# Optimization experiments

Measured on AMD Instinct MI355X. Metric: run time of the kernel, lower is better.

Reference implementation:

```python
import jax, jax.numpy as jnp
import numpy as np

K = 32          # neighbors per point (SelectorConfig)
N_DEG = 3       # radial polynomial degree
L_DEG = 3       # theta degree
M_DEG = 3       # phi degree
NP = 16384
CI = 64
CO = 64
EPS = 1e-8


def setup_inputs() -> dict:
    key = jax.random.key(0)
    k1, k2, k3 = jax.random.split(key, 3)
    position_matrix = jax.random.normal(k1, (NP, 3), dtype=jnp.float32)
    channel_matrix = jax.random.normal(k2, (NP, CI), dtype=jnp.float32)
    B = N_DEG * L_DEG * M_DEG
    coeff = jax.random.normal(k3, (B, CI, CO), dtype=jnp.float32) * 0.05
    return {"position_matrix": position_matrix,
            "channel_matrix": channel_matrix,
            "coeff": coeff}


def _knn_indices(pos):
    # brute-force kNN: (Np, Np) squared distances, top-K smallest
    sq = jnp.sum(pos * pos, axis=1)
    d2 = sq[:, None] + sq[None, :] - 2.0 * (pos @ pos.T)  # (Np, Np)
    _, idx = jax.lax.top_k(-d2, K)                        # (Np, K), includes self
    return idx


def _local_spherical(pos, idx, use_pca=True):
    nbr = pos[idx]                                  # (Np, K, 3) gather
    centers = jnp.mean(nbr, axis=1, keepdims=True)  # (Np, 1, 3)
    local = nbr - centers                           # (Np, K, 3)
    cov = jnp.einsum('nki,nkj->nij', local, local) / K   # (Np, 3, 3)
    eigvals, eigvecs = jnp.linalg.eigh(cov)         # ascending
    eigvals = eigvals[:, ::-1]                      # descending
    eigvecs = eigvecs[:, :, ::-1]
    if use_pca:
        local = jnp.einsum('nki,nij->nkj', local, eigvecs)  # rotate into PCA frame
    x, y, z = local[..., 0], local[..., 1], local[..., 2]
    r = jnp.sqrt(jnp.sum(local * local, axis=-1) + EPS)     # (Np, K)
    theta = jnp.arccos(jnp.clip(z / r, -1.0 + 1e-6, 1.0 - 1e-6))
    phi = jnp.arctan2(y, x)
    return r, theta, phi, centers, eigvals


def _poly_basis(r, theta, phi):
    # basis[n,k,b] = r^i * cos(j*theta) * cos(m*phi),  b = (i,j,m) flattened
    pr = r[..., None] ** jnp.arange(N_DEG, dtype=r.dtype)              # (Np,K,N)
    ct = jnp.cos(theta[..., None] * jnp.arange(L_DEG, dtype=r.dtype))  # (Np,K,L)
    cp = jnp.cos(phi[..., None] * jnp.arange(M_DEG, dtype=r.dtype))    # (Np,K,M)
    basis = jnp.einsum('nka,nkb,nkc->nkabc', pr, ct, cp)
    return basis.reshape(r.shape[0], r.shape[1], N_DEG * L_DEG * M_DEG)


def reference(position_matrix, channel_matrix, coeff):
    idx = _knn_indices(position_matrix)                   # (Np, K)
    r, theta, phi, _, _ = _local_spherical(position_matrix, idx, use_pca=True)
    basis = _poly_basis(r, theta, phi)                    # (Np, K, B)
    feats = channel_matrix[idx]                           # (Np, K, Ci) gather
    # fused kernel-weight construction + weighted aggregation:
    # out[o,n] = (1/K) * sum_{k,b,i} basis[n,k,b] * coeff[b,i,o] * feats[n,k,i]
    out = jnp.einsum('nkb,bio,nki->on', basis, coeff, feats) / K  # (Co, Np)
    return out
```

## Files before the change

kernel.cpp:

```cpp
#include <hip/hip_runtime.h>
#include <math.h>

#define NPOINTS 16384
#define KNN     32
#define NBASIS  27

typedef unsigned long long ull;


__device__ __forceinline__ unsigned fkey(float f) {
  unsigned u = __float_as_uint(f);
  unsigned m = (unsigned)((int)u >> 31) | 0x80000000u;
  return u ^ m;
}

__device__ __forceinline__ ull shflx64(ull v, int mask) {
  int lo = __shfl_xor((int)(unsigned)(v & 0xFFFFFFFFULL), mask, 64);
  int hi = __shfl_xor((int)(unsigned)(v >> 32), mask, 64);
  return ((ull)(unsigned)hi << 32) | (ull)(unsigned)lo;
}

__device__ __forceinline__ unsigned prefix64(ull m) {
  return __builtin_amdgcn_mbcnt_hi((unsigned)(m >> 32),
         __builtin_amdgcn_mbcnt_lo((unsigned)m, 0u));
}


__device__ __forceinline__ void slartg_dev(double f, double g, double* c, double* s, double* r) {
#pragma clang fp contract(off)
  if (g == 0.0) { *c = 1.0; *s = 0.0; *r = f; }
  else if (f == 0.0) { *c = 0.0; *s = (g >= 0.0 ? 1.0 : -1.0); *r = fabs(g); }
  else {
    double d = sqrt(f * f + g * g);
    *c = fabs(f) / d;
    *r = (f >= 0.0) ? d : -d;
    *s = g / (*r);
  }
}

__device__ __forceinline__ void slaev2_dev(double a, double b, double c,
                                           double* rt1, double* rt2, double* cs1, double* sn1) {
#pragma clang fp contract(off)
  double sm = a + c, df = a - c, adf = fabs(df), tb = b + b, ab = fabs(tb);
  double acmx, acmn;
  if (fabs(a) > fabs(c)) { acmx = a; acmn = c; } else { acmx = c; acmn = a; }
  double rt;
  if (adf > ab)      rt = adf * sqrt(1.0 + (ab / adf) * (ab / adf));
  else if (adf < ab) rt = ab * sqrt(1.0 + (adf / ab) * (adf / ab));
  else               rt = ab * sqrt(2.0);
  int sgn1;
  if (sm < 0.0) { *rt1 = 0.5 * (sm - rt); sgn1 = -1; *rt2 = (acmx / *rt1) * acmn - (b / *rt1) * b; }
  else if (sm > 0.0) { *rt1 = 0.5 * (sm + rt); sgn1 = 1; *rt2 = (acmx / *rt1) * acmn - (b / *rt1) * b; }
  else { *rt1 = 0.5 * rt; *rt2 = -0.5 * rt; sgn1 = 1; }
  int sgn2; double cs;
  if (df >= 0.0) { cs = df + rt; sgn2 = 1; } else { cs = df - rt; sgn2 = -1; }
  double acs = fabs(cs);
  if (acs > ab) { double ct = -tb / cs; double sn = 1.0 / sqrt(1.0 + ct * ct); *sn1 = sn; *cs1 = ct * sn; }
  else {
    if (ab == 0.0) { *cs1 = 1.0; *sn1 = 0.0; }
    else { double tn = -cs / tb; double c1 = 1.0 / sqrt(1.0 + tn * tn); *cs1 = c1; *sn1 = tn * c1; }
  }
  if (sgn1 == sgn2) { double tn = *cs1; *cs1 = -(*sn1); *sn1 = tn; }
}

__device__ void eigh3(float A00, float A10, float A20, float A11, float A21, float A22,
                      float V[3][3]) {
#pragma clang fp contract(off)
  const double EPS    = 5.9604644775390625e-08;
  const double EPS2   = EPS * EPS;
  const double SAFMIN = 1.1754943508222875e-38;
  double d[3], e[2];
  double tau = 0.0, v2 = 0.0;
  {
    double alpha = (double)A10, x = (double)A20;
    double a11 = (double)A11, a21 = (double)A21, a22 = (double)A22;
    double beta;
    if (x == 0.0) { tau = 0.0; v2 = 0.0; beta = alpha; }
    else {
      double nrm = sqrt(alpha * alpha + x * x);
      beta = (alpha >= 0.0) ? -nrm : nrm;
      tau = (beta - alpha) / beta;
      v2 = x / (alpha - beta);
    }
    if (tau != 0.0) {
      double w0 = tau * (a11 + a21 * v2);
      double w1 = tau * (a21 + a22 * v2);
      double cc = 0.5 * tau * (w0 + w1 * v2);
      w0 -= cc; w1 -= cc * v2;
      a11 -= 2.0 * w0;
      a21 -= (v2 * w0 + w1);
      a22 -= 2.0 * v2 * w1;
    }
    d[0] = (double)A00; d[1] = a11; d[2] = a22;
    e[0] = beta; e[1] = a21;
  }
  double Z[3][3] = { {1.0, 0.0, 0.0}, {0.0, 1.0, 0.0}, {0.0, 0.0, 1.0} };
  {
    int l1 = 1, jtot = 0;
    const int nmaxit = 90;
    double wc[2], wsn[2];
    while (l1 <= 3) {
      if (l1 > 1) e[l1 - 2] = 0.0;
      int m = 3;
      for (int mm = l1; mm <= 2; ++mm) {
        double tst = fabs(e[mm - 1]);
        if (tst == 0.0) { m = mm; break; }
        if (tst <= (sqrt(fabs(d[mm - 1])) * sqrt(fabs(d[mm]))) * EPS) { e[mm - 1] = 0.0; m = mm; break; }
      }
      int l = l1, lsv = l, lend = m, lendsv = lend;
      l1 = m + 1;
      if (lend == l) continue;
      double anorm = 0.0;
      for (int i = l; i <= lend; ++i)     anorm = fmax(anorm, fabs(d[i - 1]));
      for (int i = l; i <= lend - 1; ++i) anorm = fmax(anorm, fabs(e[i - 1]));
      if (anorm == 0.0) continue;
      if (fabs(d[lend - 1]) < fabs(d[l - 1])) { lend = lsv; l = lendsv; }
      if (lend > l) {
        bool done = false;
        while (!done) {
          int mq = lend;
          for (int mm = l; mm <= lend - 1; ++mm) {
            double tst = e[mm - 1] * e[mm - 1];
            if (tst <= (EPS2 * fabs(d[mm - 1])) * fabs(d[mm]) + SAFMIN) { mq = mm; break; }
          }
          if (mq < lend) e[mq - 1] = 0.0;
          double p = d[l - 1];
          if (mq == l) { d[l - 1] = p; ++l; if (l > lend) done = true; continue; }
          if (mq == l + 1) {
            double rt1, rt2, cc, ssn;
            slaev2_dev(d[l - 1], e[l - 1], d[l], &rt1, &rt2, &cc, &ssn);
            for (int i = 0; i < 3; ++i) {
              double t = Z[i][l];
              Z[i][l]     = cc * t - ssn * Z[i][l - 1];
              Z[i][l - 1] = ssn * t + cc * Z[i][l - 1];
            }
            d[l - 1] = rt1; d[l] = rt2; e[l - 1] = 0.0;
            l += 2; if (l > lend) done = true; continue;
          }
          if (jtot >= nmaxit) break;
          ++jtot;
          double g = (d[l] - p) / (2.0 * e[l - 1]);
          double r = sqrt(g * g + 1.0);
          g = d[mq - 1] - p + e[l - 1] / (g + ((g >= 0.0) ? r : -r));
          double ssn = 1.0, cc = 1.0;
          p = 0.0;
          for (int i = mq - 1; i >= l; --i) {
            double f = ssn * e[i - 1], b = cc * e[i - 1];
            slartg_dev(g, f, &cc, &ssn, &r);
            if (i != mq - 1) e[i] = r;
            g = d[i] - p;
            r = (d[i - 1] - g) * ssn + 2.0 * cc * b;
            p = ssn * r;
            d[i] = g + p;
            g = cc * r - b;
            wc[i - 1] = cc; wsn[i - 1] = -ssn;
          }
          for (int j = mq - 1; j >= l; --j) {
            double cj = wc[j - 1], sj = wsn[j - 1];
            for (int i = 0; i < 3; ++i) {
              double t = Z[i][j];
              Z[i][j]     = cj * t - sj * Z[i][j - 1];
              Z[i][j - 1] = sj * t + cj * Z[i][j - 1];
            }
          }
          d[l - 1] -= p; e[l - 1] = g;
        }
      } else {
        bool done = false;
        while (!done) {
          int mq = lend;
          for (int mm = l; mm >= lend + 1; --mm) {
            double tst = e[mm - 2] * e[mm - 2];
            if (tst <= (EPS2 * fabs(d[mm - 1])) * fabs(d[mm - 2]) + SAFMIN) { mq = mm; break; }
          }
          if (mq > lend) e[mq - 2] = 0.0;
          double p = d[l - 1];
          if (mq == l) { d[l - 1] = p; --l; if (l < lend) done = true; continue; }
          if (mq == l - 1) {
            double rt1, rt2, cc, ssn;
            slaev2_dev(d[l - 2], e[l - 2], d[l - 1], &rt1, &rt2, &cc, &ssn);
            for (int i = 0; i < 3; ++i) {
              double t = Z[i][l - 1];
              Z[i][l - 1] = cc * t - ssn * Z[i][l - 2];
              Z[i][l - 2] = ssn * t + cc * Z[i][l - 2];
            }
            d[l - 2] = rt1; d[l - 1] = rt2; e[l - 2] = 0.0;
            l -= 2; if (l < lend) done = true; continue;
          }
          if (jtot >= nmaxit) break;
          ++jtot;
          double g = (d[l - 2] - p) / (2.0 * e[l - 2]);
          double r = sqrt(g * g + 1.0);
          g = d[mq - 1] - p + e[l - 2] / (g + ((g >= 0.0) ? r : -r));
          double ssn = 1.0, cc = 1.0;
          p = 0.0;
          for (int i = mq; i <= l - 1; ++i) {
            double f = ssn * e[i - 1], b = cc * e[i - 1];
            slartg_dev(g, f, &cc, &ssn, &r);
            if (i != mq) e[i - 2] = r;
            g = d[i - 1] - p;
            r = (d[i] - g) * ssn + 2.0 * cc * b;
            p = ssn * r;
            d[i - 1] = g + p;
            g = cc * r - b;
            wc[i - 1] = cc; wsn[i - 1] = ssn;
          }
          for (int j = mq; j <= l - 1; ++j) {
            double cj = wc[j - 1], sj = wsn[j - 1];
            for (int i = 0; i < 3; ++i) {
              double t = Z[i][j];
              Z[i][j]     = cj * t - sj * Z[i][j - 1];
              Z[i][j - 1] = sj * t + cj * Z[i][j - 1];
            }
          }
          d[l - 1] -= p; e[l - 2] = g;
        }
      }
    }
    for (int ii = 2; ii <= 3; ++ii) {
      int i0 = ii - 1, k = i0;
      double p = d[i0 - 1];
      for (int j = ii; j <= 3; ++j) if (d[j - 1] < p) { k = j; p = d[j - 1]; }
      if (k != i0) {
        d[k - 1] = d[i0 - 1]; d[i0 - 1] = p;
        for (int rr = 0; rr < 3; ++rr) { double t = Z[rr][i0 - 1]; Z[rr][i0 - 1] = Z[rr][k - 1]; Z[rr][k - 1] = t; }
      }
    }
  }
  if (tau != 0.0) {
    for (int j = 0; j < 3; ++j) {
      double w = Z[1][j] + v2 * Z[2][j];
      Z[1][j] -= tau * w;
      Z[2][j] -= tau * v2 * w;
    }
  }
  for (int i = 0; i < 3; ++i)
    for (int j = 0; j < 3; ++j)
      V[i][j] = (float)Z[i][2 - j];
}

__global__ __launch_bounds__(256) void pack_kernel(const float* __restrict__ pos,
                                                   float4* __restrict__ pos4) {
#pragma clang fp contract(off)
  int i = blockIdx.x * 256 + threadIdx.x;
  if (i < NPOINTS) {
    float x = pos[3 * i + 0], y = pos[3 * i + 1], z = pos[3 * i + 2];
    float sq = (x * x + y * y) + z * z;
    pos4[i] = make_float4(x, y, z, sq);
  }
}

#define WPB  4
#define RPW  2
#define TPTS 512
#define NTIL (NPOINTS / TPTS)
#define CAP  128

__global__ __launch_bounds__(256) void knn_kernel(const float4* __restrict__ pos4,
                                                  unsigned* __restrict__ idx_out) {
#pragma clang fp contract(off)
  __shared__ float4 tile[TPTS];
  __shared__ ull cand[WPB][RPW][CAP];
  __shared__ ull sel[WPB][RPW][KNN];
  const int tid  = threadIdx.x;
  const int lane = tid & 63;
  const int wave = tid >> 6;
  const int rowbase = (blockIdx.x * WPB + wave) * RPW;
  const float INF = __int_as_float(0x7f800000);

  float rx[RPW], ry[RPW], rz[RPW], rq[RPW];
#pragma unroll
  for (int r = 0; r < RPW; ++r) {
    const float4 rp = pos4[rowbase + r];
    rx[r] = rp.x; ry[r] = rp.y; rz[r] = rp.z; rq[r] = rp.w;
  }

  float4 s0 = pos4[0 * 256 + tid];
  float4 s1 = pos4[1 * 256 + tid];

  float ka[RPW], kb[RPW];
#pragma unroll
  for (int r = 0; r < RPW; ++r) { ka[r] = INF; kb[r] = INF; }
  for (int t = 0; t < NTIL; ++t) {
    __syncthreads();
    tile[0 * 256 + tid] = s0;
    tile[1 * 256 + tid] = s1;
    __syncthreads();
    if (t + 1 < NTIL) {
      const int base = (t + 1) * TPTS + tid;
      s0 = pos4[base + 0 * 256];
      s1 = pos4[base + 1 * 256];
    }
#pragma unroll 2
    for (int ch = 0; ch < TPTS / 64; ch += 2) {
      const float4 p0 = tile[ch * 64 + lane];
      const float4 p1 = tile[(ch + 1) * 64 + lane];
#pragma unroll
      for (int r = 0; r < RPW; ++r) {
        const float md0 = __builtin_fmaf(rz[r], p0.z, __builtin_fmaf(ry[r], p0.y, rx[r] * p0.x));
        const float d20 = (rq[r] + p0.w) - 2.0f * md0;
        ka[r] = fminf(ka[r], d20);
        const float md1 = __builtin_fmaf(rz[r], p1.z, __builtin_fmaf(ry[r], p1.y, rx[r] * p1.x));
        const float d21 = (rq[r] + p1.w) - 2.0f * md1;
        kb[r] = fminf(kb[r], d21);
      }
    }
  }

  float Ttf[RPW];
#pragma unroll
  for (int r = 0; r < RPW; ++r) {
    float k1f = fminf(ka[r], kb[r]);
    int head = 0;
    float T = 0.f;
    for (int it = 0; it < KNN; ++it) {
      float v = (head == 0) ? k1f : INF;
      float m = v;
      for (int off = 1; off < 64; off <<= 1) {
        float o = __shfl_xor(m, off, 64);
        m = fminf(m, o);
      }
      ull win = __ballot(v == m);
      int wl = __ffsll((long long)win) - 1;
      if (lane == wl) ++head;
      T = m;
    }
    Ttf[r] = T;
  }

  s0 = pos4[0 * 256 + tid];
  s1 = pos4[1 * 256 + tid];
  unsigned cnt0 = 0, cnt1 = 0;
  const float T0 = Ttf[0], T1 = Ttf[1];
  for (int t = 0; t < NTIL; ++t) {
    __syncthreads();
    tile[0 * 256 + tid] = s0;
    tile[1 * 256 + tid] = s1;
    __syncthreads();
    if (t + 1 < NTIL) {
      const int base = (t + 1) * TPTS + tid;
      s0 = pos4[base + 0 * 256];
      s1 = pos4[base + 1 * 256];
    }
#pragma unroll 2
    for (int ch = 0; ch < TPTS / 64; ++ch) {
      const int j = t * TPTS + ch * 64 + lane;
      const float4 p = tile[ch * 64 + lane];
      const float md0 = __builtin_fmaf(rz[0], p.z, __builtin_fmaf(ry[0], p.y, rx[0] * p.x));
      const float d20 = (rq[0] + p.w) - 2.0f * md0;
      const float md1 = __builtin_fmaf(rz[1], p.z, __builtin_fmaf(ry[1], p.y, rx[1] * p.x));
      const float d21 = (rq[1] + p.w) - 2.0f * md1;
      const bool c0 = (d20 <= T0);
      const bool c1 = (d21 <= T1);
      if (__any(c0 || c1)) {
        const ull m0 = __ballot(c0);
        if (c0) {
          unsigned slot = cnt0 + prefix64(m0);
          if (slot < CAP)
            cand[wave][0][slot] = ((ull)fkey(d20) << 32) | (ull)(0xFFFFFFFFu - (unsigned)j);
        }
        cnt0 += (unsigned)__popcll(m0);
        const ull m1 = __ballot(c1);
        if (c1) {
          unsigned slot = cnt1 + prefix64(m1);
          if (slot < CAP)
            cand[wave][1][slot] = ((ull)fkey(d21) << 32) | (ull)(0xFFFFFFFFu - (unsigned)j);
        }
        cnt1 += (unsigned)__popcll(m1);
      }
    }
  }
  __builtin_amdgcn_s_waitcnt(0);

  unsigned cnt[RPW];
  cnt[0] = cnt0; cnt[1] = cnt1;
#pragma unroll
  for (int r = 0; r < RPW; ++r) {
    if (cnt[r] <= (unsigned)CAP) {
      ull c0v = (lane < (int)cnt[r]) ? cand[wave][r][lane] : ~0ULL;
      ull c1v = ((lane + 64) < (int)cnt[r]) ? cand[wave][r][lane + 64] : ~0ULL;
      ull lo = (c0v < c1v) ? c0v : c1v;
      ull hi = (c0v < c1v) ? c1v : c0v;
      int head = 0;
      for (int it = 0; it < KNN; ++it) {
        ull v = (head == 0) ? lo : ((head == 1) ? hi : ~0ULL);
        ull m = v;
        for (int off = 1; off < 64; off <<= 1) {
          ull o = shflx64(m, off);
          m = (o < m) ? o : m;
        }
        ull win = __ballot(v == m);
        int wl = __ffsll((long long)win) - 1;
        if (lane == wl) ++head;
        if (lane == 0) sel[wave][r][it] = m;
      }
    } else {
      if (lane == 0) {
        int n2 = 0;
        for (int j = 0; j < NPOINTS; ++j) {
          const float4 p = pos4[j];
          const float mdot = __builtin_fmaf(rz[r], p.z, __builtin_fmaf(ry[r], p.y, rx[r] * p.x));
          const float d2 = (rq[r] + p.w) - 2.0f * mdot;
          const unsigned key = fkey(d2);
          const ull C = ((ull)key << 32) | (ull)(0xFFFFFFFFu - (unsigned)j);
          if (n2 < KNN) {
            int b = n2 - 1;
            while (b >= 0 && sel[wave][r][b] > C) { sel[wave][r][b + 1] = sel[wave][r][b]; --b; }
            sel[wave][r][b + 1] = C;
            ++n2;
          } else if (C < sel[wave][r][KNN - 1]) {
            int b = KNN - 2;
            while (b >= 0 && sel[wave][r][b] > C) { sel[wave][r][b + 1] = sel[wave][r][b]; --b; }
            sel[wave][r][b + 1] = C;
          }
        }
      }
    }
  }
  __builtin_amdgcn_s_waitcnt(0);

  if (lane == 0) {
#pragma unroll
    for (int r = 0; r < RPW; ++r) {
      unsigned kk[KNN], ii[KNN];
      for (int a = 0; a < KNN; ++a) {
        ull C = sel[wave][r][a];
        kk[a] = (unsigned)(C >> 32);
        ii[a] = 0xFFFFFFFFu - (unsigned)(C & 0xFFFFFFFFULL);
      }
      int a = 0;
      while (a < KNN) {
        int b = a;
        while (b + 1 < KNN && kk[b + 1] == kk[a]) ++b;
        for (int x = a, y = b; x < y; ++x, --y) { unsigned tmp = ii[x]; ii[x] = ii[y]; ii[y] = tmp; }
        a = b + 1;
      }
      unsigned ob = (unsigned)(rowbase + r) * KNN;
      for (int q = 0; q < KNN; ++q) idx_out[ob + q] = ii[q];
    }
  }
}

__global__ __launch_bounds__(64) void pca_kernel(const float4* __restrict__ pos4,
                                                 const unsigned* __restrict__ idx,
                                                 float* __restrict__ center,
                                                 float* __restrict__ Vmat) {
#pragma clang fp contract(off)
  int n = blockIdx.x * 64 + threadIdx.x;
  if (n >= NPOINTS) return;
  float sx = 0.f, sy = 0.f, sz = 0.f;
  for (int k = 0; k < KNN; ++k) {
    unsigned j = idx[n * KNN + k];
    const float4 p = pos4[j];
    sx += p.x; sy += p.y; sz += p.z;
  }
  float cx = sx * 0.03125f, cy = sy * 0.03125f, cz = sz * 0.03125f;
  float c00 = 0.f, c10 = 0.f, c20 = 0.f, c11 = 0.f, c21 = 0.f, c22 = 0.f;
  for (int k = 0; k < KNN; ++k) {
    unsigned j = idx[n * KNN + k];
    const float4 p = pos4[j];
    float lx = p.x - cx;
    float ly = p.y - cy;
    float lz = p.z - cz;
    c00 += lx * lx; c10 += lx * ly; c20 += lx * lz;
    c11 += ly * ly; c21 += ly * lz; c22 += lz * lz;
  }
  c00 *= 0.03125f; c10 *= 0.03125f; c20 *= 0.03125f;
  c11 *= 0.03125f; c21 *= 0.03125f; c22 *= 0.03125f;
  float V[3][3];
  eigh3(c00, c10, c20, c11, c21, c22, V);
  center[n * 3 + 0] = cx; center[n * 3 + 1] = cy; center[n * 3 + 2] = cz;
  for (int i = 0; i < 3; ++i)
    for (int j2 = 0; j2 < 3; ++j2)
      Vmat[n * 9 + i * 3 + j2] = V[i][j2];
}

#define NT 4
__global__ __launch_bounds__(256) void conv_kernel(const float4* __restrict__ pos4,
                                                   const float* __restrict__ chan,
                                                   const float* __restrict__ coeff,
                                                   const unsigned* __restrict__ idx,
                                                   const float* __restrict__ center,
                                                   const float* __restrict__ Vmat,
                                                   float* __restrict__ out) {
#pragma clang fp contract(off)
  __shared__ float G[NT][NBASIS][64];
  __shared__ float Tsh[NT][64];
  const int tid  = threadIdx.x;
  const int lane = tid & 63;
  const int wave = tid >> 6;
  const int n0 = blockIdx.x * NT;
  const int n  = n0 + wave;

  {
    const float cx = center[n * 3 + 0], cy = center[n * 3 + 1], cz = center[n * 3 + 2];
    const float V00 = Vmat[n * 9 + 0], V01 = Vmat[n * 9 + 1], V02 = Vmat[n * 9 + 2];
    const float V10 = Vmat[n * 9 + 3], V11 = Vmat[n * 9 + 4], V12 = Vmat[n * 9 + 5];
    const float V20 = Vmat[n * 9 + 6], V21 = Vmat[n * 9 + 7], V22 = Vmat[n * 9 + 8];
    float g[NBASIS];
#pragma unroll
    for (int b = 0; b < NBASIS; ++b) g[b] = 0.f;
    for (int k = 0; k < KNN; ++k) {
      const unsigned j = idx[n * KNN + k];
      const float4 pj = pos4[j];
      const float lx = pj.x - cx;
      const float ly = pj.y - cy;
      const float lz = pj.z - cz;
      const float X  = lx * V00 + ly * V10 + lz * V20;
      const float Y  = lx * V01 + ly * V11 + lz * V21;
      const float Zc = lx * V02 + ly * V12 + lz * V22;
      const float r = sqrtf(((X * X + Y * Y) + Zc * Zc) + 1e-8f);
      float u = Zc / r;
      u = fminf(fmaxf(u, -0.999999f), 0.999999f);
      const float ct1 = u, ct2 = 2.f * u * u - 1.f;
      const float rho2 = X * X + Y * Y;
      const float cp1 = (rho2 > 0.f) ? (X / sqrtf(rho2)) : 1.f;
      const float cp2 = 2.f * cp1 * cp1 - 1.f;
      const float f = chan[(size_t)j * 64 + lane];
      const float pr1 = r, pr2 = r * r;
      float tc[9];
      tc[0] = 1.f; tc[1] = cp1; tc[2] = cp2;
      tc[3] = ct1; tc[4] = ct1 * cp1; tc[5] = ct1 * cp2;
      tc[6] = ct2; tc[7] = ct2 * cp1; tc[8] = ct2 * cp2;
#pragma unroll
      for (int m9 = 0; m9 < 9; ++m9) {
        g[m9]      = __builtin_fmaf(tc[m9],       f, g[m9]);
        g[9 + m9]  = __builtin_fmaf(pr1 * tc[m9], f, g[9 + m9]);
        g[18 + m9] = __builtin_fmaf(pr2 * tc[m9], f, g[18 + m9]);
      }
    }
#pragma unroll
    for (int b = 0; b < NBASIS; ++b) G[wave][b][lane] = g[b];
  }
  __syncthreads();

  float acc0 = 0.f;
  for (int b = 0; b < NBASIS; ++b) {
    const float4* g0p = (const float4*)(&G[wave][b][0]);
    const float* cp = coeff + (size_t)(b * 64) * 64 + lane;
#pragma unroll 4
    for (int i4 = 0; i4 < 16; ++i4) {
      const float4 g0 = g0p[i4];
      const float c0 = cp[(i4 * 4 + 0) * 64];
      const float c1 = cp[(i4 * 4 + 1) * 64];
      const float c2 = cp[(i4 * 4 + 2) * 64];
      const float c3 = cp[(i4 * 4 + 3) * 64];
      acc0 = __builtin_fmaf(c0, g0.x, acc0);
      acc0 = __builtin_fmaf(c1, g0.y, acc0);
      acc0 = __builtin_fmaf(c2, g0.z, acc0);
      acc0 = __builtin_fmaf(c3, g0.w, acc0);
    }
  }
  __syncthreads();
  Tsh[wave][lane] = acc0 * 0.03125f;
  __syncthreads();
  {
    const int o = tid >> 2, nn = tid & 3;
    out[(size_t)o * NPOINTS + (n0 + nn)] = Tsh[nn][o];
  }
}

extern "C" void kernel_launch(void* const* d_in, const int* in_sizes, int n_in,
                              void* d_out, int out_size, void* d_ws, size_t ws_size,
                              hipStream_t stream) {
  (void)in_sizes; (void)n_in; (void)out_size; (void)ws_size;
  const float* pos   = (const float*)d_in[0];
  const float* chan  = (const float*)d_in[1];
  const float* coeff = (const float*)d_in[2];
  float* out = (float*)d_out;
  unsigned char* ws = (unsigned char*)d_ws;
  float4*   pos4   = (float4*)(ws);
  unsigned* idx    = (unsigned*)(ws + (size_t)NPOINTS * 16);
  float*    center = (float*)(ws + (size_t)NPOINTS * 16 + (size_t)NPOINTS * KNN * 4);
  float*    Vmat   = (float*)(ws + (size_t)NPOINTS * 16 + (size_t)NPOINTS * KNN * 4
                              + (size_t)NPOINTS * 12);
  hipLaunchKernelGGL(pack_kernel, dim3(NPOINTS / 256),         dim3(256), 0, stream, pos, pos4);
  hipLaunchKernelGGL(knn_kernel,  dim3(NPOINTS / (WPB * RPW)), dim3(256), 0, stream, pos4, idx);
  hipLaunchKernelGGL(pca_kernel,  dim3(NPOINTS / 64),          dim3(64),  0, stream, pos4, idx, center, Vmat);
  hipLaunchKernelGGL(conv_kernel, dim3(NPOINTS / NT),          dim3(256), 0, stream, pos4, chan, coeff, idx, center, Vmat, out);
}
```

Baseline: 683.0 us.

## Split coeff contraction across waves by input channel to reuse coeff loads

The second-stage contraction is repartitioned: each wave now handles a 16-channel slice of the input dimension for all four points in the block, instead of all 64 channels for one point. Each coeff value loaded from global memory is reused across four points, cutting coeff traffic per block by four. Partial sums go through a new shared buffer and are reduced across waves, which adds one shared-memory pass and changes the floating-point summation order.

```diff
diff --git a/kernel.cpp b/kernel.cpp
--- a/kernel.cpp
+++ b/kernel.cpp
@@ -485,6 +485,7 @@
                                                    float* __restrict__ out) {
 #pragma clang fp contract(off)
   __shared__ float G[NT][NBASIS][64];
+  __shared__ float P[NT][NT][64];
   __shared__ float Tsh[NT][64];
   const int tid  = threadIdx.x;
   const int lane = tid & 63;
@@ -534,25 +535,44 @@
   }
   __syncthreads();
 
-  float acc0 = 0.f;
+  float a0 = 0.f, a1 = 0.f, a2 = 0.f, a3 = 0.f;
   for (int b = 0; b < NBASIS; ++b) {
-    const float4* g0p = (const float4*)(&G[wave][b][0]);
-    const float* cp = coeff + (size_t)(b * 64) * 64 + lane;
-#pragma unroll 4
-    for (int i4 = 0; i4 < 16; ++i4) {
-      const float4 g0 = g0p[i4];
+    const float4* g0p = (const float4*)(&G[0][b][wave * 16]);
+    const float4* g1p = (const float4*)(&G[1][b][wave * 16]);
+    const float4* g2p = (const float4*)(&G[2][b][wave * 16]);
+    const float4* g3p = (const float4*)(&G[3][b][wave * 16]);
+    const float* cp = coeff + (size_t)(b * 64 + wave * 16) * 64 + lane;
+#pragma unroll
+    for (int i4 = 0; i4 < 4; ++i4) {
       const float c0 = cp[(i4 * 4 + 0) * 64];
       const float c1 = cp[(i4 * 4 + 1) * 64];
       const float c2 = cp[(i4 * 4 + 2) * 64];
       const float c3 = cp[(i4 * 4 + 3) * 64];
-      acc0 = __builtin_fmaf(c0, g0.x, acc0);
-      acc0 = __builtin_fmaf(c1, g0.y, acc0);
-      acc0 = __builtin_fmaf(c2, g0.z, acc0);
-      acc0 = __builtin_fmaf(c3, g0.w, acc0);
-    }
-  }
+      const float4 q0 = g0p[i4];
+      const float4 q1 = g1p[i4];
+      const float4 q2 = g2p[i4];
+      const float4 q3 = g3p[i4];
+      a0 = __builtin_fmaf(c0, q0.x, a0); a0 = __builtin_fmaf(c1, q0.y, a0);
+      a0 = __builtin_fmaf(c2, q0.z, a0); a0 = __builtin_fmaf(c3, q0.w, a0);
+      a1 = __builtin_fmaf(c0, q1.x, a1); a1 = __builtin_fmaf(c1, q1.y, a1);
+      a1 = __builtin_fmaf(c2, q1.z, a1); a1 = __builtin_fmaf(c3, q1.w, a1);
+      a2 = __builtin_fmaf(c0, q2.x, a2); a2 = __builtin_fmaf(c1, q2.y, a2);
+      a2 = __builtin_fmaf(c2, q2.z, a2); a2 = __builtin_fmaf(c3, q2.w, a2);
+      a3 = __builtin_fmaf(c0, q3.x, a3); a3 = __builtin_fmaf(c1, q3.y, a3);
+      a3 = __builtin_fmaf(c2, q3.z, a3); a3 = __builtin_fmaf(c3, q3.w, a3);
+    }
+  }
+  P[wave][0][lane] = a0;
+  P[wave][1][lane] = a1;
+  P[wave][2][lane] = a2;
+  P[wave][3][lane] = a3;
   __syncthreads();
-  Tsh[wave][lane] = acc0 * 0.03125f;
+
+  {
+    const float s = ((P[0][wave][lane] + P[1][wave][lane]) +
+                     (P[2][wave][lane] + P[3][wave][lane])) * 0.03125f;
+    Tsh[wave][lane] = s;
+  }
   __syncthreads();
   {
     const int o = tid >> 2, nn = tid & 3;
```

New measurement: 614.5 us. -10.0%, faster.
